# Kernel optimization log

Hardware: AMD Instinct MI355X
Metric: run time of the kernel (lower is better)

The kernel has to match this reference:

```python
import jax, jax.numpy as jnp
import numpy as np

B, T, I, H = 512, 256, 256, 512


def _lstm(x, Wih, Whh, bih, bhh):
    # x: [B, T, I]; Wih: [4H, I]; Whh: [4H, H]; gate order i, f, g, o (torch)
    Bv = x.shape[0]
    Hv = Whh.shape[1]
    xg = jnp.einsum('bti,gi->btg', x, Wih) + bih + bhh  # [B, T, 4H] (input projections hoisted out of scan)
    xg = jnp.transpose(xg, (1, 0, 2))  # [T, B, 4H]
    h0 = jnp.zeros((Bv, Hv), x.dtype)
    c0 = jnp.zeros((Bv, Hv), x.dtype)

    def step(carry, gx):
        h, c = carry
        g = gx + h @ Whh.T  # [B, 4H]
        i, f, gg, o = jnp.split(g, 4, axis=-1)
        i = jax.nn.sigmoid(i)
        f = jax.nn.sigmoid(f)
        gg = jnp.tanh(gg)
        o = jax.nn.sigmoid(o)
        c = f * c + i * gg
        h = o * jnp.tanh(c)
        return (h, c), h

    _, hs = jax.lax.scan(step, (h0, c0), xg)  # hs: [T, B, H]
    return jnp.transpose(hs, (1, 0, 2))  # [B, T, H]


def _bn1d(x, gamma, beta, eps=1e-5):
    # torch BatchNorm1d on [N, C, L] in training mode: per-channel stats over (N, L), biased var
    m = jnp.mean(x, axis=(0, 2), keepdims=True)
    v = jnp.var(x, axis=(0, 2), keepdims=True)
    return (x - m) * jax.lax.rsqrt(v + eps) * gamma[None, :, None] + beta[None, :, None]


def setup_inputs() -> dict:
    key = jax.random.key(0)
    ks = jax.random.split(key, 14)
    s = 1.0 / np.sqrt(H)
    return {
        'x': jax.random.normal(ks[0], (B, T, I), jnp.float32),
        'Wih': jax.random.uniform(ks[1], (4 * H, I), jnp.float32, -s, s),
        'Whh': jax.random.uniform(ks[2], (4 * H, H), jnp.float32, -s, s),
        'bih': jax.random.uniform(ks[3], (4 * H,), jnp.float32, -s, s),
        'bhh': jax.random.uniform(ks[4], (4 * H,), jnp.float32, -s, s),
        'fc1_w': jax.random.uniform(ks[5], (32, H), jnp.float32, -s, s),
        'fc1_b': jax.random.uniform(ks[6], (32,), jnp.float32, -s, s),
        'fc2_w': jax.random.uniform(ks[7], (1, 32), jnp.float32, -0.17, 0.17),
        'fc2_b': jax.random.uniform(ks[8], (1,), jnp.float32, -0.17, 0.17),
        'bn1_g': jnp.ones((T,), jnp.float32),
        'bn1_b': jnp.zeros((T,), jnp.float32),
        'bn2_g': jnp.ones((T,), jnp.float32),
        'bn2_b': jnp.zeros((T,), jnp.float32),
    }


def reference(x, Wih, Whh, bih, bhh, fc1_w, fc1_b, fc2_w, fc2_b, bn1_g, bn1_b, bn2_g, bn2_b):
    lstm_out = _lstm(x, Wih, Whh, bih, bhh)  # [B, T, H]
    a = jnp.einsum('bth,oh->bto', lstm_out, fc1_w) + fc1_b  # [B, T, 32]
    a = jax.nn.leaky_relu(_bn1d(a, bn1_g, bn1_b), negative_slope=0.1)
    z = jnp.einsum('bto,po->btp', a, fc2_w) + fc2_b  # [B, T, 1]
    out = jax.nn.relu(_bn1d(z, bn2_g, bn2_b))
    return out
```

## Files before the change

kernel.cpp:

```cpp
#include <hip/hip_runtime.h>

#define BB 512
#define TT 256
#define II 256
#define HH 512

typedef __attribute__((ext_vector_type(8))) short bf16x8;
typedef __attribute__((ext_vector_type(4))) float f32x4;

__device__ __forceinline__ unsigned short f2bf(float f) {
  union { float f; unsigned u; } v; v.f = f;
  unsigned r = v.u + 0x7fffu + ((v.u >> 16) & 1u);
  return (unsigned short)(r >> 16);
}

__device__ __forceinline__ void pollw(const int* p, int t) {
  int iter = 0;
  for (;;) {
    int v = __hip_atomic_load(p, __ATOMIC_RELAXED, __HIP_MEMORY_SCOPE_AGENT);
    if (__all(v >= t)) break;
    if (++iter >= (1 << 17)) break;
    __builtin_amdgcn_s_sleep(1);
  }
}

#define OFF_CNT   0
#define OFF_HSWZ  4096
#define OFF_XSWZ  1052672ULL
#define OFF_HIST  68161536ULL
#define ZERO_WORDS 263168

__global__ void zero_k(unsigned* __restrict__ p, int n) {
  int i = blockIdx.x * blockDim.x + threadIdx.x;
  if (i < n) p[i] = 0u;
}

__global__ __launch_bounds__(256) void prep_x(const float* __restrict__ x,
                                              unsigned char* __restrict__ ws) {
  __shared__ unsigned short xs[16][264];
  const int t = blockIdx.x >> 5, rc = blockIdx.x & 31;
  const int tid = threadIdx.x;
  {
    const int r = tid >> 4, seg = tid & 15;
    const float* src = x + ((size_t)(rc * 16 + r) * TT + t) * II + seg * 16;
    const float4* s4 = (const float4*)src;
#pragma unroll
    for (int q = 0; q < 4; ++q) {
      float4 v = s4[q];
      xs[r][seg * 16 + q * 4 + 0] = f2bf(v.x);
      xs[r][seg * 16 + q * 4 + 1] = f2bf(v.y);
      xs[r][seg * 16 + q * 4 + 2] = f2bf(v.z);
      xs[r][seg * 16 + q * 4 + 3] = f2bf(v.w);
    }
  }
  __syncthreads();
  const int lane = tid & 63;
  const int row16 = lane & 15, koff = (lane >> 4) * 8;
#pragma unroll
  for (int kc = tid >> 6; kc < 8; kc += 4) {
    union { unsigned short h[8]; uint4 v; } pk;
#pragma unroll
    for (int j = 0; j < 8; ++j) pk.h[j] = xs[row16][kc * 32 + koff + j];
    *(uint4*)(ws + OFF_XSWZ + (size_t)(t * 8 + kc) * 32768u +
              ((size_t)rc * 64 + lane) * 16) = pk.v;
  }
}

__global__ __launch_bounds__(512, 2) void lstm_persist(
    const float* __restrict__ Wih, const float* __restrict__ Whh,
    const float* __restrict__ bih, const float* __restrict__ bhh,
    unsigned char* __restrict__ ws)
{
  const int gid = blockIdx.x;
  const int g = gid & 31;
  const int m = gid >> 5;
  const int tid = threadIdx.x;
  const int wv = tid >> 6, lane = tid & 63;
  const int nh = wv & 3, kh = wv >> 2;
  const int lq = lane >> 4, ln = lane & 15;

  int* flags_g = (int*)(ws + (size_t)g * 128);
  unsigned char* xswz  = ws + OFF_XSWZ;
  unsigned char* hswz0 = ws + OFF_HSWZ;
  unsigned char* hswz1 = ws + OFF_HSWZ + 524288;
  unsigned char* hist  = ws + OFF_HIST;

  const int lr3 = lane % 3;
  const int* p01  = flags_g + (lane & 1);
  const int* p234 = flags_g + 2 + lr3;
  const int* p567 = flags_g + 5 + lr3;

  bf16x8 Wf[12][4];
#pragma unroll
  for (int kk = 0; kk < 12; ++kk) {
    const int kb = (kh * 12 + kk) * 32 + lq * 8;
#pragma unroll
    for (int ns = 0; ns < 4; ++ns) {
      const int gcol = nh * 512 + m * 64 + ns * 16 + ln;
      const float* s = (kb < 256) ? (Wih + (size_t)gcol * 256 + kb)
                                  : (Whh + (size_t)gcol * 512 + (kb - 256));
      bf16x8 w;
#pragma unroll
      for (int j = 0; j < 8; ++j) w[j] = (short)f2bf(s[j]);
      Wf[kk][ns] = w;
    }
  }

  const int urow = tid >> 5;
  const int ujl  = (tid & 31) * 2;
  float bia2[2][4];
#pragma unroll
  for (int cc = 0; cc < 2; ++cc)
#pragma unroll
    for (int nt = 0; nt < 4; ++nt) {
      int gcol = nt * 512 + m * 64 + ujl + cc;
      bia2[cc][nt] = bih[gcol] + bhh[gcol];
    }

  __shared__ float g_s[8704];
  __shared__ float h_s[1088];

  float c2[2] = {0.f, 0.f};
  const f32x4 zero4 = {0.f, 0.f, 0.f, 0.f};

#pragma unroll 1
  for (int t = 0; t < 256; ++t) {
    unsigned char* hrd = (t & 1) ? hswz1 : hswz0;
    unsigned char* hwr = (t & 1) ? hswz0 : hswz1;

    f32x4 acc[4] = {zero4, zero4, zero4, zero4};
    const unsigned char* hbase = hrd + (size_t)g * 1024u + (size_t)lane * 16u;

    if (kh == 0) {
#pragma unroll
      for (int kc = 0; kc < 8; ++kc) {
        bf16x8 a = *(const bf16x8*)(xswz + (size_t)(t * 8 + kc) * 32768u +
                                    ((size_t)(g * 64 + lane)) * 16);
#pragma unroll
        for (int ns = 0; ns < 4; ++ns)
          acc[ns] = __builtin_amdgcn_mfma_f32_16x16x32_bf16(a, Wf[kc][ns], acc[ns], 0, 0, 0);
      }
      if (t > 0) { pollw(p01, t); asm volatile("" ::: "memory"); }
      unsigned long long u0[4], u1[4];
#pragma unroll
      for (int p = 0; p < 4; ++p) {
        const unsigned long long* q =
            (const unsigned long long*)(hbase + (size_t)p * 32768u);
        u0[p] = __hip_atomic_load(q + 0, __ATOMIC_RELAXED, __HIP_MEMORY_SCOPE_AGENT);
        u1[p] = __hip_atomic_load(q + 1, __ATOMIC_RELAXED, __HIP_MEMORY_SCOPE_AGENT);
      }
#pragma unroll
      for (int kk = 0; kk < 4; ++kk) {
        union { unsigned long long q[2]; bf16x8 v; } u;
        u.q[0] = u0[kk]; u.q[1] = u1[kk];
#pragma unroll
        for (int ns = 0; ns < 4; ++ns)
          acc[ns] = __builtin_amdgcn_mfma_f32_16x16x32_bf16(u.v, Wf[8 + kk][ns], acc[ns], 0, 0, 0);
      }
    } else {
      if (t > 0) { pollw(p234, t); asm volatile("" ::: "memory"); }
      unsigned long long u0[6], u1[6];
#pragma unroll
      for (int p = 0; p < 6; ++p) {
        const unsigned long long* q =
            (const unsigned long long*)(hbase + (size_t)(4 + p) * 32768u);
        u0[p] = __hip_atomic_load(q + 0, __ATOMIC_RELAXED, __HIP_MEMORY_SCOPE_AGENT);
        u1[p] = __hip_atomic_load(q + 1, __ATOMIC_RELAXED, __HIP_MEMORY_SCOPE_AGENT);
      }
      if (t > 0) { pollw(p567, t); asm volatile("" ::: "memory"); }
#pragma unroll
      for (int kk = 0; kk < 12; ++kk) {
        const int slot = kk % 6;
        union { unsigned long long q[2]; bf16x8 v; } u;
        u.q[0] = u0[slot]; u.q[1] = u1[slot];
        if (kk < 6) {
          const unsigned long long* q =
              (const unsigned long long*)(hbase + (size_t)(10 + kk) * 32768u);
          u0[slot] = __hip_atomic_load(q + 0, __ATOMIC_RELAXED, __HIP_MEMORY_SCOPE_AGENT);
          u1[slot] = __hip_atomic_load(q + 1, __ATOMIC_RELAXED, __HIP_MEMORY_SCOPE_AGENT);
        }
#pragma unroll
        for (int ns = 0; ns < 4; ++ns)
          acc[ns] = __builtin_amdgcn_mfma_f32_16x16x32_bf16(u.v, Wf[kk][ns], acc[ns], 0, 0, 0);
      }
    }
#pragma unroll
    for (int ns = 0; ns < 4; ++ns)
#pragma unroll
      for (int r = 0; r < 4; ++r)
        g_s[((kh * 16 + lq * 4 + r) * 4 + nh) * 68 + ns * 16 + ln] = acc[ns][r];
    __syncthreads();

    {
#pragma unroll
      for (int cc = 0; cc < 2; ++cc) {
        const int jl = ujl + cc;
        float gi = g_s[((0 * 16 + urow) * 4 + 0) * 68 + jl]
                 + g_s[((1 * 16 + urow) * 4 + 0) * 68 + jl] + bia2[cc][0];
        float gf = g_s[((0 * 16 + urow) * 4 + 1) * 68 + jl]
                 + g_s[((1 * 16 + urow) * 4 + 1) * 68 + jl] + bia2[cc][1];
        float gg = g_s[((0 * 16 + urow) * 4 + 2) * 68 + jl]
                 + g_s[((1 * 16 + urow) * 4 + 2) * 68 + jl] + bia2[cc][2];
        float go = g_s[((0 * 16 + urow) * 4 + 3) * 68 + jl]
                 + g_s[((1 * 16 + urow) * 4 + 3) * 68 + jl] + bia2[cc][3];
        float iv = 1.f / (1.f + __expf(-gi));
        float fv = 1.f / (1.f + __expf(-gf));
        float gv = 1.f - 2.f / (__expf(2.f * gg) + 1.f);
        float ov = 1.f / (1.f + __expf(-go));
        float cv = fv * c2[cc] + iv * gv;
        c2[cc] = cv;
        h_s[urow * 68 + jl] = ov * (1.f - 2.f / (__expf(2.f * cv) + 1.f));
      }
    }
    __syncthreads();

    if (tid < 128) {
      int cc = tid >> 6;
      int lp = tid & 63;
      union { unsigned short s[8]; uint4 v; } pk;
#pragma unroll
      for (int j = 0; j < 8; ++j)
        pk.s[j] = f2bf(h_s[(lp & 15) * 68 + cc * 32 + (lp >> 4) * 8 + j]);
      *(uint4*)(hwr + (size_t)(2 * m + cc) * 32768u + (size_t)g * 1024u +
                (size_t)lp * 16u) = pk.v;
    }
    __syncthreads();

    if (tid == 0)
      __hip_atomic_store(flags_g + m, t + 1, __ATOMIC_RELAXED,
                         __HIP_MEMORY_SCOPE_AGENT);

    if (tid < 128) {
      int row = tid >> 3, jl0 = (tid & 7) * 8;
      union { unsigned short s[8]; uint4 v; } hq;
#pragma unroll
      for (int j = 0; j < 8; ++j) hq.s[j] = f2bf(h_s[row * 68 + jl0 + j]);
      int b = g * 16 + row;
      *(uint4*)(hist + ((size_t)(b * 256 + t) * 512 + m * 64 + jl0) * 2) = hq.v;
    }
  }
}

__global__ __launch_bounds__(256) void e1_fc1(
    const float* __restrict__ fc1_w, const unsigned char* __restrict__ hist,
    float* __restrict__ a_out)
{
  const int tid = threadIdx.x, wv = tid >> 6, lane = tid & 63;
  const int lq = lane >> 4, ln = lane & 15;

  bf16x8 Bf[16][2];
#pragma unroll
  for (int kk = 0; kk < 16; ++kk) {
#pragma unroll
    for (int nt = 0; nt < 2; ++nt) {
      const float* s = fc1_w + (size_t)(nt * 16 + ln) * 512 + kk * 32 + lq * 8;
      bf16x8 w;
#pragma unroll
      for (int j = 0; j < 8; ++j) w[j] = (short)f2bf(s[j]);
      Bf[kk][nt] = w;
    }
  }

  const int rbase = blockIdx.x * 128 + wv * 32;
  const f32x4 zero4 = {0.f, 0.f, 0.f, 0.f};
  f32x4 acc[2][2] = {{zero4, zero4}, {zero4, zero4}};
#pragma unroll
  for (int kk = 0; kk < 16; ++kk) {
    bf16x8 a0 = *(const bf16x8*)(hist + ((size_t)(rbase + ln) * 512 + kk * 32 + lq * 8) * 2);
    bf16x8 a1 = *(const bf16x8*)(hist + ((size_t)(rbase + 16 + ln) * 512 + kk * 32 + lq * 8) * 2);
#pragma unroll
    for (int nt = 0; nt < 2; ++nt) {
      acc[0][nt] = __builtin_amdgcn_mfma_f32_16x16x32_bf16(a0, Bf[kk][nt], acc[0][nt], 0, 0, 0);
      acc[1][nt] = __builtin_amdgcn_mfma_f32_16x16x32_bf16(a1, Bf[kk][nt], acc[1][nt], 0, 0, 0);
    }
  }
#pragma unroll
  for (int mt = 0; mt < 2; ++mt)
#pragma unroll
    for (int nt = 0; nt < 2; ++nt)
#pragma unroll
      for (int r = 0; r < 4; ++r) {
        int row = rbase + mt * 16 + lq * 4 + r;
        a_out[(size_t)row * 32 + nt * 16 + ln] = acc[mt][nt][r];
      }
}

__global__ __launch_bounds__(256) void e2_head(
    const float* __restrict__ a_in, const float* __restrict__ fc1_b,
    const float* __restrict__ fc2_w, const float* __restrict__ fc2_b,
    const float* __restrict__ bn1_g, const float* __restrict__ bn1_b,
    const float* __restrict__ bn2_g, const float* __restrict__ bn2_b,
    float* __restrict__ out)
{
  const int t = blockIdx.x, tid = threadIdx.x;
  __shared__ float fb[32], fw[32];
  __shared__ float red[4][2], red2[4][2];
  if (tid < 32) { fb[tid] = fc1_b[tid]; fw[tid] = fc2_w[tid]; }
  __syncthreads();

  float va[2][32];
  float s1 = 0.f, s2 = 0.f;
#pragma unroll
  for (int rr = 0; rr < 2; ++rr) {
    int b = tid * 2 + rr;
    const float* p = a_in + ((size_t)b * 256 + t) * 32;
#pragma unroll
    for (int o = 0; o < 32; ++o) {
      float v = p[o] + fb[o];
      va[rr][o] = v;
      s1 += v; s2 += v * v;
    }
  }
#pragma unroll
  for (int off = 32; off > 0; off >>= 1) {
    s1 += __shfl_down(s1, off);
    s2 += __shfl_down(s2, off);
  }
  if ((tid & 63) == 0) { red[tid >> 6][0] = s1; red[tid >> 6][1] = s2; }
  __syncthreads();
  float tot1 = red[0][0] + red[1][0] + red[2][0] + red[3][0];
  float tot2 = red[0][1] + red[1][1] + red[2][1] + red[3][1];
  float m1 = tot1 * (1.f / 16384.f);
  float v1 = tot2 * (1.f / 16384.f) - m1 * m1;
  float sc1 = bn1_g[t] * rsqrtf(v1 + 1e-5f);
  float sh1 = bn1_b[t];

  float z[2];
  float zs1 = 0.f, zs2 = 0.f;
#pragma unroll
  for (int rr = 0; rr < 2; ++rr) {
    float acc = fc2_b[0];
#pragma unroll
    for (int o = 0; o < 32; ++o) {
      float av = (va[rr][o] - m1) * sc1 + sh1;
      av = (av > 0.f) ? av : 0.1f * av;
      acc += av * fw[o];
    }
    z[rr] = acc; zs1 += acc; zs2 += acc * acc;
  }
#pragma unroll
  for (int off = 32; off > 0; off >>= 1) {
    zs1 += __shfl_down(zs1, off);
    zs2 += __shfl_down(zs2, off);
  }
  if ((tid & 63) == 0) { red2[tid >> 6][0] = zs1; red2[tid >> 6][1] = zs2; }
  __syncthreads();
  float zt1 = red2[0][0] + red2[1][0] + red2[2][0] + red2[3][0];
  float zt2 = red2[0][1] + red2[1][1] + red2[2][1] + red2[3][1];
  float m2 = zt1 * (1.f / 512.f);
  float v2 = zt2 * (1.f / 512.f) - m2 * m2;
  float sc2 = bn2_g[t] * rsqrtf(v2 + 1e-5f);
  float sh2 = bn2_b[t];
#pragma unroll
  for (int rr = 0; rr < 2; ++rr) {
    int b = tid * 2 + rr;
    float res = (z[rr] - m2) * sc2 + sh2;
    out[(size_t)b * 256 + t] = (res > 0.f) ? res : 0.f;
  }
}

extern "C" void kernel_launch(void* const* d_in, const int* in_sizes, int n_in,
                              void* d_out, int out_size, void* d_ws, size_t ws_size,
                              hipStream_t stream) {
  const float* x    = (const float*)d_in[0];
  const float* Wih  = (const float*)d_in[1];
  const float* Whh  = (const float*)d_in[2];
  const float* bih  = (const float*)d_in[3];
  const float* bhh  = (const float*)d_in[4];
  const float* fc1w = (const float*)d_in[5];
  const float* fc1b = (const float*)d_in[6];
  const float* fc2w = (const float*)d_in[7];
  const float* fc2b = (const float*)d_in[8];
  const float* b1g  = (const float*)d_in[9];
  const float* b1b  = (const float*)d_in[10];
  const float* b2g  = (const float*)d_in[11];
  const float* b2b  = (const float*)d_in[12];
  unsigned char* ws = (unsigned char*)d_ws;
  float* out = (float*)d_out;
  float* a_buf = (float*)(ws + OFF_XSWZ);

  zero_k<<<1028, 256, 0, stream>>>((unsigned*)ws, ZERO_WORDS);
  prep_x<<<8192, 256, 0, stream>>>(x, ws);
  lstm_persist<<<256, 512, 0, stream>>>(Wih, Whh, bih, bhh, ws);
  e1_fc1<<<1024, 256, 0, stream>>>(fc1w, ws + OFF_HIST, a_buf);
  e2_head<<<256, 256, 0, stream>>>(a_buf, fc1b, fc2w, fc2b, b1g, b1b, b2g, b2b, out);
}
```

Measured before the change: 1.412 ms.

## Fuse fc1 projection into persistent LSTM kernel using streamed h fragments

Folds the fc1 matmul into the recurrent kernel. Blocks with m==0 reuse the h_{t-1} bf16 fragments they already load for the recurrence and run extra MFMAs against fc1 weights held in shared memory, then write the fc1 output for step t-1. A tail pass after the loop handles the last timestep. This removes the separate e1_fc1 kernel and the bf16 hidden-state history writes and reads to global memory. In exchange it adds work and a larger shared-memory footprint (about 40KB more) to every block on the serial critical path, which may affect occupancy at 2 blocks per CU.

```diff
diff --git a/kernel.cpp b/kernel.cpp
--- a/kernel.cpp
+++ b/kernel.cpp
@@ -69,7 +69,7 @@
 __global__ __launch_bounds__(512, 2) void lstm_persist(
     const float* __restrict__ Wih, const float* __restrict__ Whh,
     const float* __restrict__ bih, const float* __restrict__ bhh,
-    unsigned char* __restrict__ ws)
+    const float* __restrict__ fc1_w, unsigned char* __restrict__ ws)
 {
   const int gid = blockIdx.x;
   const int g = gid & 31;
@@ -83,7 +83,7 @@
   unsigned char* xswz  = ws + OFF_XSWZ;
   unsigned char* hswz0 = ws + OFF_HSWZ;
   unsigned char* hswz1 = ws + OFF_HSWZ + 524288;
-  unsigned char* hist  = ws + OFF_HIST;
+  float* a_out = (float*)(ws + OFF_HIST);
 
   const int lr3 = lane % 3;
   const int* p01  = flags_g + (lane & 1);
@@ -119,6 +119,21 @@
 
   __shared__ float g_s[8704];
   __shared__ float h_s[1088];
+  __shared__ bf16x8 fc1f[2048];
+  __shared__ float fpart[2048];
+
+#pragma unroll
+  for (int i = 0; i < 4; ++i) {
+    int s = tid + i * 512;
+    int chunk = s >> 7, tile = (s >> 6) & 1, lnn = s & 63;
+    int col = tile * 16 + (lnn & 15);
+    int kb2 = chunk * 32 + (lnn >> 4) * 8;
+    bf16x8 w;
+#pragma unroll
+    for (int j = 0; j < 8; ++j) w[j] = (short)f2bf(fc1_w[(size_t)col * 512 + kb2 + j]);
+    fc1f[chunk * 128 + tile * 64 + lnn] = w;
+  }
+  __syncthreads();
 
   float c2[2] = {0.f, 0.f};
   const f32x4 zero4 = {0.f, 0.f, 0.f, 0.f};
@@ -129,6 +144,7 @@
     unsigned char* hwr = (t & 1) ? hswz0 : hswz1;
 
     f32x4 acc[4] = {zero4, zero4, zero4, zero4};
+    f32x4 accf[2] = {zero4, zero4};
     const unsigned char* hbase = hrd + (size_t)g * 1024u + (size_t)lane * 16u;
 
     if (kh == 0) {
@@ -156,6 +172,10 @@
 #pragma unroll
         for (int ns = 0; ns < 4; ++ns)
           acc[ns] = __builtin_amdgcn_mfma_f32_16x16x32_bf16(u.v, Wf[8 + kk][ns], acc[ns], 0, 0, 0);
+        if (nh == 0) {
+          accf[0] = __builtin_amdgcn_mfma_f32_16x16x32_bf16(u.v, fc1f[kk * 128 + lane], accf[0], 0, 0, 0);
+          accf[1] = __builtin_amdgcn_mfma_f32_16x16x32_bf16(u.v, fc1f[kk * 128 + 64 + lane], accf[1], 0, 0, 0);
+        }
       }
     } else {
       if (t > 0) { pollw(p234, t); asm volatile("" ::: "memory"); }
@@ -182,6 +202,10 @@
 #pragma unroll
         for (int ns = 0; ns < 4; ++ns)
           acc[ns] = __builtin_amdgcn_mfma_f32_16x16x32_bf16(u.v, Wf[kk][ns], acc[ns], 0, 0, 0);
+        if (nh == 0) {
+          accf[0] = __builtin_amdgcn_mfma_f32_16x16x32_bf16(u.v, fc1f[(4 + kk) * 128 + lane], accf[0], 0, 0, 0);
+          accf[1] = __builtin_amdgcn_mfma_f32_16x16x32_bf16(u.v, fc1f[(4 + kk) * 128 + 64 + lane], accf[1], 0, 0, 0);
+        }
       }
     }
 #pragma unroll
@@ -189,6 +213,13 @@
 #pragma unroll
       for (int r = 0; r < 4; ++r)
         g_s[((kh * 16 + lq * 4 + r) * 4 + nh) * 68 + ns * 16 + ln] = acc[ns][r];
+    if (nh == 0) {
+#pragma unroll
+      for (int tile = 0; tile < 2; ++tile)
+#pragma unroll
+        for (int r = 0; r < 4; ++r)
+          fpart[(((t & 1) * 2 + kh) * 2 + tile) * 256 + (lq * 4 + r) * 16 + ln] = accf[tile][r];
+    }
     __syncthreads();
 
     {
@@ -230,59 +261,46 @@
       __hip_atomic_store(flags_g + m, t + 1, __ATOMIC_RELAXED,
                          __HIP_MEMORY_SCOPE_AGENT);
 
-    if (tid < 128) {
-      int row = tid >> 3, jl0 = (tid & 7) * 8;
-      union { unsigned short s[8]; uint4 v; } hq;
-#pragma unroll
-      for (int j = 0; j < 8; ++j) hq.s[j] = f2bf(h_s[row * 68 + jl0 + j]);
-      int b = g * 16 + row;
-      *(uint4*)(hist + ((size_t)(b * 256 + t) * 512 + m * 64 + jl0) * 2) = hq.v;
-    }
-  }
-}
-
-__global__ __launch_bounds__(256) void e1_fc1(
-    const float* __restrict__ fc1_w, const unsigned char* __restrict__ hist,
-    float* __restrict__ a_out)
-{
-  const int tid = threadIdx.x, wv = tid >> 6, lane = tid & 63;
-  const int lq = lane >> 4, ln = lane & 15;
-
-  bf16x8 Bf[16][2];
-#pragma unroll
-  for (int kk = 0; kk < 16; ++kk) {
-#pragma unroll
-    for (int nt = 0; nt < 2; ++nt) {
-      const float* s = fc1_w + (size_t)(nt * 16 + ln) * 512 + kk * 32 + lq * 8;
-      bf16x8 w;
-#pragma unroll
-      for (int j = 0; j < 8; ++j) w[j] = (short)f2bf(s[j]);
-      Bf[kk][nt] = w;
-    }
-  }
-
-  const int rbase = blockIdx.x * 128 + wv * 32;
-  const f32x4 zero4 = {0.f, 0.f, 0.f, 0.f};
-  f32x4 acc[2][2] = {{zero4, zero4}, {zero4, zero4}};
-#pragma unroll
-  for (int kk = 0; kk < 16; ++kk) {
-    bf16x8 a0 = *(const bf16x8*)(hist + ((size_t)(rbase + ln) * 512 + kk * 32 + lq * 8) * 2);
-    bf16x8 a1 = *(const bf16x8*)(hist + ((size_t)(rbase + 16 + ln) * 512 + kk * 32 + lq * 8) * 2);
-#pragma unroll
-    for (int nt = 0; nt < 2; ++nt) {
-      acc[0][nt] = __builtin_amdgcn_mfma_f32_16x16x32_bf16(a0, Bf[kk][nt], acc[0][nt], 0, 0, 0);
-      acc[1][nt] = __builtin_amdgcn_mfma_f32_16x16x32_bf16(a1, Bf[kk][nt], acc[1][nt], 0, 0, 0);
-    }
-  }
-#pragma unroll
-  for (int mt = 0; mt < 2; ++mt)
-#pragma unroll
-    for (int nt = 0; nt < 2; ++nt)
-#pragma unroll
-      for (int r = 0; r < 4; ++r) {
-        int row = rbase + mt * 16 + lq * 4 + r;
-        a_out[(size_t)row * 32 + nt * 16 + ln] = acc[mt][nt][r];
-      }
+    if (m == 0 && t > 0) {
+      int row = tid >> 5, col = tid & 31;
+      int tile = col >> 4, cl = col & 15;
+      float v = fpart[(((t & 1) * 2 + 0) * 2 + tile) * 256 + row * 16 + cl]
+              + fpart[(((t & 1) * 2 + 1) * 2 + tile) * 256 + row * 16 + cl];
+      a_out[((size_t)(g * 16 + row) * 256 + (t - 1)) * 32 + col] = v;
+    }
+  }
+
+  if (nh == 0) {
+    pollw(flags_g + (lane & 7), 256);
+    asm volatile("" ::: "memory");
+    const unsigned char* hbase = hswz0 + (size_t)g * 1024u + (size_t)lane * 16u;
+    f32x4 accf[2] = {zero4, zero4};
+    const int c0 = (kh == 0) ? 0 : 4;
+    const int cn = (kh == 0) ? 4 : 12;
+    for (int kk = 0; kk < cn; ++kk) {
+      const int ch = c0 + kk;
+      const unsigned long long* q =
+          (const unsigned long long*)(hbase + (size_t)ch * 32768u);
+      union { unsigned long long qq[2]; bf16x8 v; } u;
+      u.qq[0] = __hip_atomic_load(q + 0, __ATOMIC_RELAXED, __HIP_MEMORY_SCOPE_AGENT);
+      u.qq[1] = __hip_atomic_load(q + 1, __ATOMIC_RELAXED, __HIP_MEMORY_SCOPE_AGENT);
+      accf[0] = __builtin_amdgcn_mfma_f32_16x16x32_bf16(u.v, fc1f[ch * 128 + lane], accf[0], 0, 0, 0);
+      accf[1] = __builtin_amdgcn_mfma_f32_16x16x32_bf16(u.v, fc1f[ch * 128 + 64 + lane], accf[1], 0, 0, 0);
+    }
+#pragma unroll
+    for (int tile = 0; tile < 2; ++tile)
+#pragma unroll
+      for (int r = 0; r < 4; ++r)
+        fpart[((0 * 2 + kh) * 2 + tile) * 256 + (lq * 4 + r) * 16 + ln] = accf[tile][r];
+  }
+  __syncthreads();
+  if (m == 0) {
+    int row = tid >> 5, col = tid & 31;
+    int tile = col >> 4, cl = col & 15;
+    float v = fpart[((0 * 2 + 0) * 2 + tile) * 256 + row * 16 + cl]
+            + fpart[((0 * 2 + 1) * 2 + tile) * 256 + row * 16 + cl];
+    a_out[((size_t)(g * 16 + row) * 256 + 255) * 32 + col] = v;
+  }
 }
 
 __global__ __launch_bounds__(256) void e2_head(
@@ -377,11 +395,10 @@
   const float* b2b  = (const float*)d_in[12];
   unsigned char* ws = (unsigned char*)d_ws;
   float* out = (float*)d_out;
-  float* a_buf = (float*)(ws + OFF_XSWZ);
+  float* a_buf = (float*)(ws + OFF_HIST);
 
   zero_k<<<1028, 256, 0, stream>>>((unsigned*)ws, ZERO_WORDS);
   prep_x<<<8192, 256, 0, stream>>>(x, ws);
-  lstm_persist<<<256, 512, 0, stream>>>(Wih, Whh, bih, bhh, ws);
-  e1_fc1<<<1024, 256, 0, stream>>>(fc1w, ws + OFF_HIST, a_buf);
+  lstm_persist<<<256, 512, 0, stream>>>(Wih, Whh, bih, bhh, fc1w, ws);
   e2_head<<<256, 256, 0, stream>>>(a_buf, fc1b, fc2w, fc2b, b1g, b1b, b2g, b2b, out);
 }
```

New measurement: 1.717 ms. +21.6%, slower.
